# Kernel optimization log

Measured on AMD Instinct MI355X. Metric: run time of the kernel, lower is better.

## Reference

```python
import jax, jax.numpy as jnp
import numpy as np

K, R, KAPPA = 4, 16384, 32
NX, NF, DOUT = 3, 13, 64


def setup_inputs() -> dict:
    key = jax.random.key(0)
    ks = jax.random.split(key, 6)
    X = jax.random.normal(ks[0], (K, R, NX), dtype=jnp.float32)
    F = jax.random.normal(ks[1], (K, R, NF), dtype=jnp.float32)
    N = jax.random.randint(ks[2], (K, R, KAPPA), 0, R, dtype=jnp.int32)
    H = jax.random.normal(ks[3], (DOUT, NX + NF), dtype=jnp.float32) * 0.1
    gamma = jax.random.normal(ks[4], (DOUT, DOUT), dtype=jnp.float32) * 0.1
    gamma_bias = jax.random.normal(ks[5], (DOUT,), dtype=jnp.float32) * 0.1
    return {"X": X, "F": F, "N": N, "H": H, "gamma": gamma, "gamma_bias": gamma_bias}


def reference(X, F, N, H, gamma, gamma_bias):
    # P = [X | F] : [K, R, n]
    P = jnp.concatenate([X, F], axis=2)
    # batched gather (tf.gather batch_dims=1): P_groups[k, r, i, :] = P[k, N[k, r, i], :]
    P_groups = jax.vmap(lambda p, n: p[n])(P, N)  # [K, R, kappa, n]
    # SharedMLP: P_groups @ H^T, then relu (H_activation)
    PHT = jax.nn.relu(jnp.einsum('krin,dn->krid', P_groups, H))
    # component-wise max over neighbors
    PHT_max = jnp.max(PHT, axis=2)  # [K, R, Dout]
    # Dense: (P* Gamma) + bias, then relu (gamma_activation)
    Y = jnp.einsum('krd,de->kre', PHT_max, gamma) + gamma_bias
    return jax.nn.relu(Y)
```

## Files before the change

### kernel.cpp

```cpp
#include <hip/hip_runtime.h>
#include <hip/hip_fp16.h>
#include <math.h>

#define KR 65536
#define RS 16384
#define KAPPA 32

typedef __attribute__((ext_vector_type(8))) _Float16 f16x8;
typedef __attribute__((ext_vector_type(4))) float f32x4;
typedef __attribute__((ext_vector_type(16))) float f32x16;

__global__ __launch_bounds__(256) void pack_kernel(
    const float* __restrict__ X, const float* __restrict__ F,
    const float* __restrict__ H, _Float16* __restrict__ Pp,
    _Float16* __restrict__ Hp) {
  const int p = blockIdx.x * 256 + threadIdx.x;
  const size_t qx = (size_t)p * 3, qf = (size_t)p * 13;
  f16x8 lo, hi;
  lo[0] = (_Float16)X[qx + 0];
  lo[1] = (_Float16)X[qx + 1];
  lo[2] = (_Float16)X[qx + 2];
  #pragma unroll
  for (int j = 0; j < 5; ++j) lo[3 + j] = (_Float16)F[qf + j];
  #pragma unroll
  for (int j = 0; j < 8; ++j) hi[j] = (_Float16)F[qf + 5 + j];
  *(f16x8*)(Pp + (size_t)p * 16 + 0) = lo;
  *(f16x8*)(Pp + (size_t)p * 16 + 8) = hi;

  if (blockIdx.x == 0 && threadIdx.x < 64) {
    const int d = threadIdx.x;
    f16x8 a, b;
    #pragma unroll
    for (int j = 0; j < 8; ++j) {
      a[j] = (_Float16)H[d * 16 + j];
      b[j] = (_Float16)H[d * 16 + 8 + j];
    }
    *(f16x8*)(Hp + d * 16 + 0) = a;
    *(f16x8*)(Hp + d * 16 + 8) = b;
  }
}

__global__ __launch_bounds__(256) void fused_kernel(
    const _Float16* __restrict__ Pp, const _Float16* __restrict__ Hp,
    const int* __restrict__ N, const float* __restrict__ gamma,
    const float* __restrict__ gbias, float* __restrict__ Y) {
  __shared__ _Float16 Gt[64 * 72];
  __shared__ _Float16 Ml[32 * 72];
  __shared__ float Bl[64];

  const int t = threadIdx.x;
  #pragma unroll
  for (int ii = 0; ii < 4; ++ii) {
    const int i = t + ii * 256;
    const float4 gv = ((const float4*)gamma)[i];
    const int d = i >> 4, e0 = (i & 15) * 4;
    Gt[(e0 + 0) * 72 + d] = (_Float16)gv.x;
    Gt[(e0 + 1) * 72 + d] = (_Float16)gv.y;
    Gt[(e0 + 2) * 72 + d] = (_Float16)gv.z;
    Gt[(e0 + 3) * 72 + d] = (_Float16)gv.w;
  }
  if (t < 64) Bl[t] = gbias[t];

  const int lane = t & 63, wave = t >> 6;
  const int l31 = lane & 31, hsel = lane >> 5;

  const int base = blockIdx.x * 32;
  const int k = blockIdx.x >> 9;
  const _Float16* Pk = Pp + ((size_t)k * RS) * 16;

  const f16x8 hb0 = *(const f16x8*)(Hp + (0  + l31) * 16 + hsel * 8);
  const f16x8 hb1 = *(const f16x8*)(Hp + (32 + l31) * 16 + hsel * 8);

  const int p0 = base + wave * 8;
  int idx[8];
  #pragma unroll
  for (int j = 0; j < 8; ++j)
    idx[j] = __builtin_nontemporal_load(N + (size_t)(p0 + j) * KAPPA + l31);

  const f32x16 z = {0.f, 0.f, 0.f, 0.f, 0.f, 0.f, 0.f, 0.f,
                    0.f, 0.f, 0.f, 0.f, 0.f, 0.f, 0.f, 0.f};
  #pragma unroll
  for (int j = 0; j < 8; ++j) {
    const f16x8 a = *(const f16x8*)(Pk + (size_t)idx[j] * 16 + hsel * 8);
    const f32x16 c0 = __builtin_amdgcn_mfma_f32_32x32x16_f16(a, hb0, z, 0, 0, 0);
    const f32x16 c1 = __builtin_amdgcn_mfma_f32_32x32x16_f16(a, hb1, z, 0, 0, 0);
    float m0 = fmaxf(
        fmaxf(fmaxf(fmaxf(c0[0], c0[1]), fmaxf(c0[2], c0[3])),
              fmaxf(fmaxf(c0[4], c0[5]), fmaxf(c0[6], c0[7]))),
        fmaxf(fmaxf(fmaxf(c0[8], c0[9]), fmaxf(c0[10], c0[11])),
              fmaxf(fmaxf(c0[12], c0[13]), fmaxf(c0[14], c0[15]))));
    float m1 = fmaxf(
        fmaxf(fmaxf(fmaxf(c1[0], c1[1]), fmaxf(c1[2], c1[3])),
              fmaxf(fmaxf(c1[4], c1[5]), fmaxf(c1[6], c1[7]))),
        fmaxf(fmaxf(fmaxf(c1[8], c1[9]), fmaxf(c1[10], c1[11])),
              fmaxf(fmaxf(c1[12], c1[13]), fmaxf(c1[14], c1[15]))));
    m0 = fmaxf(m0, 0.0f);
    m1 = fmaxf(m1, 0.0f);
    m0 = fmaxf(m0, __shfl_xor(m0, 32, 64));
    m1 = fmaxf(m1, __shfl_xor(m1, 32, 64));
    const float ms = hsel ? m1 : m0;
    Ml[(wave * 8 + j) * 72 + lane] = (_Float16)ms;
  }
  __syncthreads();

  const int ln15 = lane & 15, quad = lane >> 4;
  const int rt = wave & 1, ct = wave >> 1;
  f32x4 acc[2] = {{0.f, 0.f, 0.f, 0.f}, {0.f, 0.f, 0.f, 0.f}};
  #pragma unroll
  for (int ks = 0; ks < 2; ++ks) {
    const f16x8 af = *(const f16x8*)(Ml + (rt * 16 + ln15) * 72 + ks * 32 + quad * 8);
    #pragma unroll
    for (int nt = 0; nt < 2; ++nt) {
      const f16x8 bf = *(const f16x8*)(Gt + (ct * 32 + nt * 16 + ln15) * 72 + ks * 32 + quad * 8);
      acc[nt] = __builtin_amdgcn_mfma_f32_16x16x32_f16(af, bf, acc[nt], 0, 0, 0);
    }
  }

  #pragma unroll
  for (int nt = 0; nt < 2; ++nt) {
    const float bv = Bl[ct * 32 + nt * 16 + ln15];
    #pragma unroll
    for (int r = 0; r < 4; ++r) {
      const float y = fmaxf(acc[nt][r] + bv, 0.0f);
      __builtin_nontemporal_store(
          y, Y + (size_t)(base + rt * 16 + quad * 4 + r) * 64 + ct * 32 + nt * 16 + ln15);
    }
  }
}

extern "C" void kernel_launch(void* const* d_in, const int* in_sizes, int n_in,
                              void* d_out, int out_size, void* d_ws, size_t ws_size,
                              hipStream_t stream) {
  const float* X  = (const float*)d_in[0];
  const float* F  = (const float*)d_in[1];
  const int*   N  = (const int*)d_in[2];
  const float* H  = (const float*)d_in[3];
  const float* G  = (const float*)d_in[4];
  const float* Gb = (const float*)d_in[5];
  float* Y = (float*)d_out;
  _Float16* Pp = (_Float16*)d_ws;
  _Float16* Hp = Pp + (size_t)KR * 16;

  pack_kernel<<<256, 256, 0, stream>>>(X, F, H, Pp, Hp);
  fused_kernel<<<2048, 256, 0, stream>>>(Pp, Hp, N, G, Gb, Y);
}
```

Before: 95.51 us.

## Pretranspose gamma to fp16 once and process 64 points per block

Gamma is now converted to fp16 and transposed once in the pack kernel, so each fused block just copies it into shared memory with vector loads instead of doing scattered fp32-to-fp16 transposes. Each block now handles 64 points in two halves of 8 per wave, which halves the grid and amortizes the gamma/bias setup over more work. Each wave computes a full 16x64 output tile in the dense stage. The tradeoff is fewer blocks in flight and a serialized gather loop per wave, which may reduce latency hiding for the random neighbor gathers.

```diff
diff --git a/kernel.cpp b/kernel.cpp
--- a/kernel.cpp
+++ b/kernel.cpp
@@ -12,8 +12,9 @@
 
 __global__ __launch_bounds__(256) void pack_kernel(
     const float* __restrict__ X, const float* __restrict__ F,
-    const float* __restrict__ H, _Float16* __restrict__ Pp,
-    _Float16* __restrict__ Hp) {
+    const float* __restrict__ H, const float* __restrict__ gamma,
+    _Float16* __restrict__ Pp, _Float16* __restrict__ Hp,
+    _Float16* __restrict__ Gp) {
   const int p = blockIdx.x * 256 + threadIdx.x;
   const size_t qx = (size_t)p * 3, qf = (size_t)p * 13;
   f16x8 lo, hi;
@@ -27,103 +28,107 @@
   *(f16x8*)(Pp + (size_t)p * 16 + 0) = lo;
   *(f16x8*)(Pp + (size_t)p * 16 + 8) = hi;
 
-  if (blockIdx.x == 0 && threadIdx.x < 64) {
-    const int d = threadIdx.x;
-    f16x8 a, b;
-    #pragma unroll
-    for (int j = 0; j < 8; ++j) {
-      a[j] = (_Float16)H[d * 16 + j];
-      b[j] = (_Float16)H[d * 16 + 8 + j];
+  if (blockIdx.x == 0) {
+    if (threadIdx.x < 64) {
+      const int d = threadIdx.x;
+      f16x8 a, b;
+      #pragma unroll
+      for (int j = 0; j < 8; ++j) {
+        a[j] = (_Float16)H[d * 16 + j];
+        b[j] = (_Float16)H[d * 16 + 8 + j];
+      }
+      *(f16x8*)(Hp + d * 16 + 0) = a;
+      *(f16x8*)(Hp + d * 16 + 8) = b;
     }
-    *(f16x8*)(Hp + d * 16 + 0) = a;
-    *(f16x8*)(Hp + d * 16 + 8) = b;
+    for (int i = threadIdx.x; i < 4096; i += 256) {
+      const int d = i >> 6, e = i & 63;
+      Gp[e * 64 + d] = (_Float16)gamma[i];
+    }
   }
+}
+
+__device__ __forceinline__ float max16(const f32x16 c) {
+  const float a = fmaxf(fmaxf(c[0], c[1]), c[2]);
+  const float b = fmaxf(fmaxf(c[3], c[4]), c[5]);
+  const float d = fmaxf(fmaxf(c[6], c[7]), c[8]);
+  const float e = fmaxf(fmaxf(c[9], c[10]), c[11]);
+  const float f = fmaxf(fmaxf(c[12], c[13]), c[14]);
+  return fmaxf(fmaxf(fmaxf(a, b), d), fmaxf(fmaxf(e, f), c[15]));
 }
 
 __global__ __launch_bounds__(256) void fused_kernel(
     const _Float16* __restrict__ Pp, const _Float16* __restrict__ Hp,
-    const int* __restrict__ N, const float* __restrict__ gamma,
+    const _Float16* __restrict__ Gp, const int* __restrict__ N,
     const float* __restrict__ gbias, float* __restrict__ Y) {
   __shared__ _Float16 Gt[64 * 72];
-  __shared__ _Float16 Ml[32 * 72];
+  __shared__ _Float16 Ml[64 * 72];
   __shared__ float Bl[64];
 
   const int t = threadIdx.x;
   #pragma unroll
-  for (int ii = 0; ii < 4; ++ii) {
-    const int i = t + ii * 256;
-    const float4 gv = ((const float4*)gamma)[i];
-    const int d = i >> 4, e0 = (i & 15) * 4;
-    Gt[(e0 + 0) * 72 + d] = (_Float16)gv.x;
-    Gt[(e0 + 1) * 72 + d] = (_Float16)gv.y;
-    Gt[(e0 + 2) * 72 + d] = (_Float16)gv.z;
-    Gt[(e0 + 3) * 72 + d] = (_Float16)gv.w;
+  for (int u = 0; u < 2; ++u) {
+    const int ci = t * 2 + u;
+    const f16x8 g = *(const f16x8*)(Gp + ci * 8);
+    *(f16x8*)(Gt + (ci >> 3) * 72 + (ci & 7) * 8) = g;
   }
   if (t < 64) Bl[t] = gbias[t];
 
   const int lane = t & 63, wave = t >> 6;
   const int l31 = lane & 31, hsel = lane >> 5;
 
-  const int base = blockIdx.x * 32;
-  const int k = blockIdx.x >> 9;
+  const int base = blockIdx.x * 64;
+  const int k = blockIdx.x >> 8;
   const _Float16* Pk = Pp + ((size_t)k * RS) * 16;
 
   const f16x8 hb0 = *(const f16x8*)(Hp + (0  + l31) * 16 + hsel * 8);
   const f16x8 hb1 = *(const f16x8*)(Hp + (32 + l31) * 16 + hsel * 8);
 
-  const int p0 = base + wave * 8;
-  int idx[8];
-  #pragma unroll
-  for (int j = 0; j < 8; ++j)
-    idx[j] = __builtin_nontemporal_load(N + (size_t)(p0 + j) * KAPPA + l31);
-
   const f32x16 z = {0.f, 0.f, 0.f, 0.f, 0.f, 0.f, 0.f, 0.f,
                     0.f, 0.f, 0.f, 0.f, 0.f, 0.f, 0.f, 0.f};
-  #pragma unroll
-  for (int j = 0; j < 8; ++j) {
-    const f16x8 a = *(const f16x8*)(Pk + (size_t)idx[j] * 16 + hsel * 8);
-    const f32x16 c0 = __builtin_amdgcn_mfma_f32_32x32x16_f16(a, hb0, z, 0, 0, 0);
-    const f32x16 c1 = __builtin_amdgcn_mfma_f32_32x32x16_f16(a, hb1, z, 0, 0, 0);
-    float m0 = fmaxf(
-        fmaxf(fmaxf(fmaxf(c0[0], c0[1]), fmaxf(c0[2], c0[3])),
-              fmaxf(fmaxf(c0[4], c0[5]), fmaxf(c0[6], c0[7]))),
-        fmaxf(fmaxf(fmaxf(c0[8], c0[9]), fmaxf(c0[10], c0[11])),
-              fmaxf(fmaxf(c0[12], c0[13]), fmaxf(c0[14], c0[15]))));
-    float m1 = fmaxf(
-        fmaxf(fmaxf(fmaxf(c1[0], c1[1]), fmaxf(c1[2], c1[3])),
-              fmaxf(fmaxf(c1[4], c1[5]), fmaxf(c1[6], c1[7]))),
-        fmaxf(fmaxf(fmaxf(c1[8], c1[9]), fmaxf(c1[10], c1[11])),
-              fmaxf(fmaxf(c1[12], c1[13]), fmaxf(c1[14], c1[15]))));
-    m0 = fmaxf(m0, 0.0f);
-    m1 = fmaxf(m1, 0.0f);
-    m0 = fmaxf(m0, __shfl_xor(m0, 32, 64));
-    m1 = fmaxf(m1, __shfl_xor(m1, 32, 64));
-    const float ms = hsel ? m1 : m0;
-    Ml[(wave * 8 + j) * 72 + lane] = (_Float16)ms;
+
+  #pragma unroll 1
+  for (int half = 0; half < 2; ++half) {
+    const int p0 = base + wave * 16 + half * 8;
+    int idx[8];
+    #pragma unroll
+    for (int j = 0; j < 8; ++j)
+      idx[j] = __builtin_nontemporal_load(N + (size_t)(p0 + j) * KAPPA + l31);
+
+    #pragma unroll
+    for (int j = 0; j < 8; ++j) {
+      const f16x8 a = *(const f16x8*)(Pk + (size_t)idx[j] * 16 + hsel * 8);
+      const f32x16 c0 = __builtin_amdgcn_mfma_f32_32x32x16_f16(a, hb0, z, 0, 0, 0);
+      const f32x16 c1 = __builtin_amdgcn_mfma_f32_32x32x16_f16(a, hb1, z, 0, 0, 0);
+      float m0 = fmaxf(max16(c0), 0.0f);
+      float m1 = fmaxf(max16(c1), 0.0f);
+      m0 = fmaxf(m0, __shfl_xor(m0, 32, 64));
+      m1 = fmaxf(m1, __shfl_xor(m1, 32, 64));
+      Ml[(wave * 16 + half * 8 + j) * 72 + lane] = (_Float16)(hsel ? m1 : m0);
+    }
   }
   __syncthreads();
 
   const int ln15 = lane & 15, quad = lane >> 4;
-  const int rt = wave & 1, ct = wave >> 1;
-  f32x4 acc[2] = {{0.f, 0.f, 0.f, 0.f}, {0.f, 0.f, 0.f, 0.f}};
+  f32x4 acc[4] = {{0.f, 0.f, 0.f, 0.f}, {0.f, 0.f, 0.f, 0.f},
+                  {0.f, 0.f, 0.f, 0.f}, {0.f, 0.f, 0.f, 0.f}};
   #pragma unroll
   for (int ks = 0; ks < 2; ++ks) {
-    const f16x8 af = *(const f16x8*)(Ml + (rt * 16 + ln15) * 72 + ks * 32 + quad * 8);
+    const f16x8 af = *(const f16x8*)(Ml + (wave * 16 + ln15) * 72 + ks * 32 + quad * 8);
     #pragma unroll
-    for (int nt = 0; nt < 2; ++nt) {
-      const f16x8 bf = *(const f16x8*)(Gt + (ct * 32 + nt * 16 + ln15) * 72 + ks * 32 + quad * 8);
+    for (int nt = 0; nt < 4; ++nt) {
+      const f16x8 bf = *(const f16x8*)(Gt + (nt * 16 + ln15) * 72 + ks * 32 + quad * 8);
       acc[nt] = __builtin_amdgcn_mfma_f32_16x16x32_f16(af, bf, acc[nt], 0, 0, 0);
     }
   }
 
   #pragma unroll
-  for (int nt = 0; nt < 2; ++nt) {
-    const float bv = Bl[ct * 32 + nt * 16 + ln15];
+  for (int nt = 0; nt < 4; ++nt) {
+    const float bv = Bl[nt * 16 + ln15];
     #pragma unroll
     for (int r = 0; r < 4; ++r) {
       const float y = fmaxf(acc[nt][r] + bv, 0.0f);
       __builtin_nontemporal_store(
-          y, Y + (size_t)(base + rt * 16 + quad * 4 + r) * 64 + ct * 32 + nt * 16 + ln15);
+          y, Y + (size_t)(base + wave * 16 + quad * 4 + r) * 64 + nt * 16 + ln15);
     }
   }
 }
@@ -140,7 +145,8 @@
   float* Y = (float*)d_out;
   _Float16* Pp = (_Float16*)d_ws;
   _Float16* Hp = Pp + (size_t)KR * 16;
+  _Float16* Gp = Hp + 64 * 16;
 
-  pack_kernel<<<256, 256, 0, stream>>>(X, F, H, Pp, Hp);
-  fused_kernel<<<2048, 256, 0, stream>>>(Pp, Hp, N, G, Gb, Y);
+  pack_kernel<<<256, 256, 0, stream>>>(X, F, H, G, Pp, Hp, Gp);
+  fused_kernel<<<1024, 256, 0, stream>>>(Pp, Hp, Gp, N, Gb, Y);
 }
```

After: 94.37 us. Within noise of the previous version (-1.2%).
